# Kernel optimization log

Hardware: AMD Instinct MI355X
Metric: run time of the kernel (lower is better)

## Reference

```python
import jax, jax.numpy as jnp
import numpy as np
from jax import lax

N_TRIALS = 4096
N_T = 2000
DT = 0.001
LEAK_RATE = 0.01      # leak=True
TIME_CONSTANT = 0.01  # time_dependence=True
VARIANCE = 1.0


def setup_inputs() -> dict:
    key = jax.random.key(0)
    k1, k2 = jax.random.split(key)
    stimulus = jax.random.normal(k1, (N_TRIALS, N_T), dtype=jnp.float32)
    noise = jax.random.normal(k2, (N_TRIALS, N_T), dtype=jnp.float32)
    return {
        "stimulus": stimulus,
        "noise": noise,
        "a": jnp.float32(2.0),
        "z": jnp.float32(0.5),
        "drift_gain": jnp.float32(7.0),
        "drift_offset": jnp.float32(0.0),
        "beta": jnp.float32(50.0),
    }


def reference(stimulus, noise, a, z, drift_gain, drift_offset, beta):
    n_trials, n_t = stimulus.shape
    starting_point = z * a
    drift_rates = drift_gain * stimulus + drift_offset
    scaled_noise = noise * jnp.sqrt(jnp.float32(VARIANCE * DT))
    # evidence[t] = decay * evidence[t-1] + u[t-1]
    # where decay = 1 - leak_rate*dt (constant) and
    # u[i] = drift[i]*dt + noise[i] + leak_rate*starting_point*dt
    decay = jnp.float32(1.0 - LEAK_RATE * DT)
    u = drift_rates * DT + scaled_noise + LEAK_RATE * starting_point * DT  # (n_trials, n_t)

    def step(e_prev, u_t):
        e_new = decay * e_prev + u_t
        return e_new, e_new

    e0 = starting_point * jnp.ones((n_trials,), dtype=stimulus.dtype)
    # steps t=1..n_t-1 consume u[:, t-1]
    _, ev_rest = lax.scan(step, e0, jnp.swapaxes(u[:, : n_t - 1], 0, 1))  # (n_t-1, n_trials)
    evidence = jnp.concatenate([e0[None, :], ev_rest], axis=0).T  # (n_trials, n_t)

    urgency = jnp.arange(n_t, dtype=stimulus.dtype) * TIME_CONSTANT  # (n_t,)
    dv = urgency[None, :] * (evidence - starting_point) + starting_point
    h1 = jax.nn.sigmoid(beta * (dv - a))
    h0 = jax.nn.sigmoid(-beta * dv)
    return dv, h1, h0
```

## Files before the change

### kernel.cpp

```cpp
#include <hip/hip_runtime.h>
#include <math.h>

#define N_T   2000
#define NG    500
#define WAVES 4

__global__ __launch_bounds__(256) void ddm_kernel(
    const float* __restrict__ stim,
    const float* __restrict__ noise,
    const float* __restrict__ a_p,
    const float* __restrict__ z_p,
    const float* __restrict__ gain_p,
    const float* __restrict__ off_p,
    const float* __restrict__ beta_p,
    float* __restrict__ out,
    int n_trials)
{
    const int wave  = threadIdx.x >> 6;
    const int lane  = threadIdx.x & 63;
    const int trial = blockIdx.x * WAVES + wave;
    if (trial >= n_trials) return;

    constexpr float DT   = 0.001f;
    constexpr float LEAK = 0.01f;
    constexpr float DEC  = 1.0f - LEAK * DT;
    constexpr float INV  = 1.0f / DEC;
    constexpr float De2 = DEC * DEC, De3 = De2 * DEC, De4 = De2 * De2;
    constexpr float I2  = INV * INV, I3  = I2 * INV, I4  = I2 * I2;
    constexpr float D8 = De4 * De4, D16 = D8 * D8, D32 = D16 * D16,
                    D64 = D32 * D32, D128 = D64 * D64, D256 = D128 * D128;
    constexpr float I8 = I4 * I4, I16 = I8 * I8, I32 = I16 * I16,
                    I64 = I32 * I32, I128 = I64 * I64, I256 = I128 * I128;

    const float a    = *a_p;
    const float z    = *z_p;
    const float gain = *gain_p;
    const float offs = *off_p;
    const float beta = *beta_p;

    const float sp = z * a;
    const float C1 = gain * DT;
    const float C2 = sqrtf(1.0f * DT);
    const float C3 = offs * DT + LEAK * sp * DT;

    float dl = 1.f, il = 1.f, bd = De4, bi = I4;
    int nb = lane;
#pragma unroll
    for (int b = 0; b < 6; ++b) {
        if (nb & 1) { dl *= bd; il *= bi; }
        bd *= bd; bi *= bi; nb >>= 1;
    }
    il *= INV;

    const float* srow = stim  + (size_t)trial * N_T;
    const float* nrow = noise + (size_t)trial * N_T;
    float* dv_out = out;
    float* h1_out = out + (size_t)n_trials * N_T;
    float* h0_out = out + 2 * (size_t)n_trials * N_T;
    const size_t rbase = (size_t)trial * N_T;

    float carry = 0.f;
    float dpj = dl;
    float ifj = il;

    float4 s_cur = *(const float4*)(srow + 4 * lane);
    float4 n_cur = *(const float4*)(nrow + 4 * lane);

#pragma unroll
    for (int j = 0; j < 8; ++j) {
        float4 s_nxt = make_float4(0.f, 0.f, 0.f, 0.f);
        float4 n_nxt = make_float4(0.f, 0.f, 0.f, 0.f);
        if (j < 7) {
            const int g2 = (j + 1) * 64 + lane;
            if (g2 < NG) {
                s_nxt = *(const float4*)(srow + 4 * g2);
                n_nxt = *(const float4*)(nrow + 4 * g2);
            }
        }

        const int  g     = j * 64 + lane;
        const bool valid = g < NG;
        const float m    = valid ? 1.f : 0.f;
        const int  t0    = 4 * g;

        const float u0 = C1 * s_cur.x + C2 * n_cur.x + C3;
        const float u1 = C1 * s_cur.y + C2 * n_cur.y + C3;
        const float u2 = C1 * s_cur.z + C2 * n_cur.z + C3;
        const float u3 = C1 * s_cur.w + C2 * n_cur.w + C3;

        const float w0 = u0 * ifj * m;
        const float w1 = u1 * (ifj * INV) * m;
        const float w2 = u2 * (ifj * I2) * m;
        const float w3 = u3 * (ifj * I3) * m;

        const float l0 = w0, l1 = l0 + w1, l2 = l1 + w2, l3 = l2 + w3;

        float sc = l3;
#pragma unroll
        for (int off = 1; off < 64; off <<= 1) {
            const float v = __shfl_up(sc, off, 64);
            sc += (lane >= off) ? v : 0.f;
        }
        const float excl = sc - l3;
        const float btot = __shfl(sc, 63, 64);
        const float S0   = carry + excl;
        carry += btot;

        const float e0 = dpj *         (sp + S0);
        const float e1 = (dpj * DEC) * (sp + S0 + l0);
        const float e2 = (dpj * De2) * (sp + S0 + l1);
        const float e3 = (dpj * De3) * (sp + S0 + l2);

        float4 dv4, h14, h04;
        dv4.x = (float)(t0    ) * 0.01f * (e0 - sp) + sp;
        dv4.y = (float)(t0 + 1) * 0.01f * (e1 - sp) + sp;
        dv4.z = (float)(t0 + 2) * 0.01f * (e2 - sp) + sp;
        dv4.w = (float)(t0 + 3) * 0.01f * (e3 - sp) + sp;
#pragma unroll
        for (int q = 0; q < 4; ++q) {
            const float dv = ((const float*)&dv4)[q];
            ((float*)&h14)[q] = __builtin_amdgcn_rcpf(1.0f + __expf(-beta * (dv - a)));
            ((float*)&h04)[q] = __builtin_amdgcn_rcpf(1.0f + __expf( beta * dv));
        }

        if (valid) {
            const size_t base = rbase + (size_t)t0;
            *(float4*)(dv_out + base) = dv4;
            *(float4*)(h1_out + base) = h14;
            *(float4*)(h0_out + base) = h04;
        }

        dpj *= D256;
        ifj *= I256;
        s_cur = s_nxt;
        n_cur = n_nxt;
    }
}

extern "C" void kernel_launch(void* const* d_in, const int* in_sizes, int n_in,
                              void* d_out, int out_size, void* d_ws, size_t ws_size,
                              hipStream_t stream) {
    const float* stim  = (const float*)d_in[0];
    const float* noise = (const float*)d_in[1];
    const float* a_p   = (const float*)d_in[2];
    const float* z_p   = (const float*)d_in[3];
    const float* g_p   = (const float*)d_in[4];
    const float* o_p   = (const float*)d_in[5];
    const float* b_p   = (const float*)d_in[6];
    float* outp = (float*)d_out;

    const int n_trials = in_sizes[0] / N_T;
    const int blocks = (n_trials + WAVES - 1) / WAVES;
    ddm_kernel<<<blocks, 256, 0, stream>>>(stim, noise, a_p, z_p, g_p, o_p, b_p,
                                           outp, n_trials);
}
```

Before: 165.0 us.

## Load all row chunks upfront and interleave eight independent wave scans

Each wave now issues all 16 float4 loads for its trial before doing any math, which replaces the one-ahead prefetch. It then runs the eight per-chunk 64-lane shuffle scans in lockstep so their shuffle latencies overlap, and resolves the cross-chunk carries afterward. This exposes more memory-level and instruction-level parallelism in exchange for higher register pressure. The launch bounds also request 4 waves per EU as an occupancy hint, and out-of-range lanes are clamped to a valid address rather than branched around.

```diff
diff --git a/kernel.cpp b/kernel.cpp
--- a/kernel.cpp
+++ b/kernel.cpp
@@ -5,7 +5,7 @@
 #define NG    500
 #define WAVES 4
 
-__global__ __launch_bounds__(256) void ddm_kernel(
+__global__ __launch_bounds__(256, 4) void ddm_kernel(
     const float* __restrict__ stim,
     const float* __restrict__ noise,
     const float* __restrict__ a_p,
@@ -54,62 +54,77 @@
 
     const float* srow = stim  + (size_t)trial * N_T;
     const float* nrow = noise + (size_t)trial * N_T;
+
+    float4 sv[8], nv[8];
+#pragma unroll
+    for (int j = 0; j < 8; ++j) {
+        const int g  = j * 64 + lane;
+        const int gc = (g < NG) ? g : (NG - 1);
+        sv[j] = *(const float4*)(srow + 4 * gc);
+        nv[j] = *(const float4*)(nrow + 4 * gc);
+    }
+
+    float l0[8], l1[8], l2[8], l3[8];
+    {
+        float ifj = il;
+#pragma unroll
+        for (int j = 0; j < 8; ++j) {
+            const float m = ((j * 64 + lane) < NG) ? 1.f : 0.f;
+            const float u0 = C1 * sv[j].x + C2 * nv[j].x + C3;
+            const float u1 = C1 * sv[j].y + C2 * nv[j].y + C3;
+            const float u2 = C1 * sv[j].z + C2 * nv[j].z + C3;
+            const float u3 = C1 * sv[j].w + C2 * nv[j].w + C3;
+            const float w0 = u0 * ifj * m;
+            const float w1 = u1 * (ifj * INV) * m;
+            const float w2 = u2 * (ifj * I2) * m;
+            const float w3 = u3 * (ifj * I3) * m;
+            l0[j] = w0;
+            l1[j] = l0[j] + w1;
+            l2[j] = l1[j] + w2;
+            l3[j] = l2[j] + w3;
+            ifj *= I256;
+        }
+    }
+
+    float sc[8];
+#pragma unroll
+    for (int j = 0; j < 8; ++j) sc[j] = l3[j];
+#pragma unroll
+    for (int off = 1; off < 64; off <<= 1) {
+        float v[8];
+#pragma unroll
+        for (int j = 0; j < 8; ++j) v[j] = __shfl_up(sc[j], off, 64);
+#pragma unroll
+        for (int j = 0; j < 8; ++j) sc[j] += (lane >= off) ? v[j] : 0.f;
+    }
+
+    float S0[8];
+    {
+        float c = 0.f;
+#pragma unroll
+        for (int j = 0; j < 8; ++j) {
+            const float btot = __shfl(sc[j], 63, 64);
+            S0[j] = c + (sc[j] - l3[j]);
+            c += btot;
+        }
+    }
+
     float* dv_out = out;
     float* h1_out = out + (size_t)n_trials * N_T;
     float* h0_out = out + 2 * (size_t)n_trials * N_T;
     const size_t rbase = (size_t)trial * N_T;
 
-    float carry = 0.f;
     float dpj = dl;
-    float ifj = il;
-
-    float4 s_cur = *(const float4*)(srow + 4 * lane);
-    float4 n_cur = *(const float4*)(nrow + 4 * lane);
-
 #pragma unroll
     for (int j = 0; j < 8; ++j) {
-        float4 s_nxt = make_float4(0.f, 0.f, 0.f, 0.f);
-        float4 n_nxt = make_float4(0.f, 0.f, 0.f, 0.f);
-        if (j < 7) {
-            const int g2 = (j + 1) * 64 + lane;
-            if (g2 < NG) {
-                s_nxt = *(const float4*)(srow + 4 * g2);
-                n_nxt = *(const float4*)(nrow + 4 * g2);
-            }
-        }
-
         const int  g     = j * 64 + lane;
         const bool valid = g < NG;
-        const float m    = valid ? 1.f : 0.f;
         const int  t0    = 4 * g;
 
-        const float u0 = C1 * s_cur.x + C2 * n_cur.x + C3;
-        const float u1 = C1 * s_cur.y + C2 * n_cur.y + C3;
-        const float u2 = C1 * s_cur.z + C2 * n_cur.z + C3;
-        const float u3 = C1 * s_cur.w + C2 * n_cur.w + C3;
-
-        const float w0 = u0 * ifj * m;
-        const float w1 = u1 * (ifj * INV) * m;
-        const float w2 = u2 * (ifj * I2) * m;
-        const float w3 = u3 * (ifj * I3) * m;
-
-        const float l0 = w0, l1 = l0 + w1, l2 = l1 + w2, l3 = l2 + w3;
-
-        float sc = l3;
-#pragma unroll
-        for (int off = 1; off < 64; off <<= 1) {
-            const float v = __shfl_up(sc, off, 64);
-            sc += (lane >= off) ? v : 0.f;
-        }
-        const float excl = sc - l3;
-        const float btot = __shfl(sc, 63, 64);
-        const float S0   = carry + excl;
-        carry += btot;
-
-        const float e0 = dpj *         (sp + S0);
-        const float e1 = (dpj * DEC) * (sp + S0 + l0);
-        const float e2 = (dpj * De2) * (sp + S0 + l1);
-        const float e3 = (dpj * De3) * (sp + S0 + l2);
+        const float e0 = dpj *         (sp + S0[j]);
+        const float e1 = (dpj * DEC) * (sp + S0[j] + l0[j]);
+        const float e2 = (dpj * De2) * (sp + S0[j] + l1[j]);
+        const float e3 = (dpj * De3) * (sp + S0[j] + l2[j]);
 
         float4 dv4, h14, h04;
         dv4.x = (float)(t0    ) * 0.01f * (e0 - sp) + sp;
@@ -129,11 +144,7 @@
             *(float4*)(h1_out + base) = h14;
             *(float4*)(h0_out + base) = h04;
         }
-
         dpj *= D256;
-        ifj *= I256;
-        s_cur = s_nxt;
-        n_cur = n_nxt;
     }
 }
 
```

After: 162.6 us. No clear change (-1.5%).
